# Performance work log

Hardware: AMD Instinct MI355X
Metric: run time of the kernel (lower is better)

The kernel has to match this reference:

```python
import jax, jax.numpy as jnp
import numpy as np

N = 500          # max_neurons, all alive
INPUT_SIZE = 3072
FEAT_DIM = 64
OUT_SIZE = 10
BATCH = 8192
RADIUS = 20.0
VOL = 100.0      # cubic volume (100,100,100)
N_ITER = 3


def setup_inputs() -> dict:
    key = jax.random.key(0)
    k_x, k_pos, k_iw, k_f, k_ow = jax.random.split(key, 5)
    x = jax.random.normal(k_x, (BATCH, INPUT_SIZE), dtype=jnp.float32)
    # seed positions spread across the volume, roughly matching _init_seeds
    positions = jax.random.uniform(k_pos, (N, 3), dtype=jnp.float32) * 80.0 + 10.0
    input_weights = jax.random.normal(k_iw, (N, INPUT_SIZE), dtype=jnp.float32) * 0.02
    features = jax.random.normal(k_f, (N, FEAT_DIM), dtype=jnp.float32) * 0.1
    output_weights = jax.random.normal(k_ow, (N, OUT_SIZE), dtype=jnp.float32) * 0.02
    biases = jnp.zeros((N,), dtype=jnp.float32)
    return {"x": x, "positions": positions, "input_weights": input_weights,
            "features": features, "output_weights": output_weights, "biases": biases}


def reference(x, positions, input_weights, features, output_weights, biases):
    # clamp positions into the volume (per-axis, vol is cubic here)
    pos = jnp.clip(positions, 0.1, VOL - 0.1)  # [N,3]

    # pairwise distances (grad-safe sqrt at the zero diagonal)
    diff = pos[:, None, :] - pos[None, :, :]          # [N,N,3]
    sq = jnp.sum(diff * diff, axis=-1)                # [N,N]
    pos_mask = sq > 0.0
    dist = jnp.where(pos_mask, jnp.sqrt(jnp.where(pos_mask, sq, 1.0)), 0.0)

    conn_mask = (dist < RADIUS) & (dist > 0.0)
    attenuation = jnp.exp(-dist / RADIUS) * conn_mask.astype(dist.dtype)

    # feature similarity (F.normalize clamps the norm from below at eps)
    feat_norm = features / jnp.maximum(
        jnp.linalg.norm(features, axis=1, keepdims=True), 1e-6)
    feat_sim = jnp.clip(feat_norm @ feat_norm.T, -1.0, 1.0)  # [N,N]

    conn_w = attenuation * (0.5 + 0.5 * feat_sim)
    conn_w = conn_w / (jnp.sum(conn_w, axis=1, keepdims=True) + 1e-6)

    # input gating: neurons near x=0 receive input
    x_norm = pos[:, 0] / VOL                          # [N]
    input_weight = jnp.exp(-2.0 * x_norm)
    input_weight = input_weight / (jnp.sum(input_weight) + 1e-6)

    activations = x @ input_weights.T * input_weight + biases  # [B,N]

    # iterative message passing (fixed small iteration count)
    for _ in range(N_ITER):
        msg = activations @ conn_w.T                  # [B,N]
        activations = jnp.minimum(jax.nn.relu(activations + 0.5 * msg), 50.0)

    # output gating: neurons near x=VOL emit output
    output_weight = jnp.exp(2.0 * (x_norm - 1.0))
    output_weight = output_weight / (jnp.sum(output_weight) + 1e-6)

    return activations @ (output_weights * output_weight[:, None])  # [B,OUT]
```

## Files before the change

### kernel.cpp

```cpp
#include <hip/hip_runtime.h>
#include <stdint.h>

#define N_REAL 500
#define NPAD   512
#define K_IN   3072
#define NBATCH 8192
#define NOUT   10
#define RADIUS 20.0f
#define VOLF   100.0f

typedef __attribute__((ext_vector_type(8))) __bf16 bf16x8;
typedef __attribute__((ext_vector_type(4))) float  f32x4;
typedef __attribute__((ext_vector_type(4))) unsigned short us4;

__device__ __forceinline__ unsigned short f2bf(float f) {
    unsigned int u = __float_as_uint(f);
    u += 0x7FFFu + ((u >> 16) & 1u);
    return (unsigned short)(u >> 16);
}
__device__ __forceinline__ float bf2f(unsigned short h) {
    return __uint_as_float(((unsigned int)h) << 16);
}
__device__ __forceinline__ uint2 cvt_pk4(float4 v) {
    uint2 r;
    asm("v_cvt_pk_bf16_f32 %0, %1, %2" : "=v"(r.x) : "v"(v.x), "v"(v.y));
    asm("v_cvt_pk_bf16_f32 %0, %1, %2" : "=v"(r.y) : "v"(v.z), "v"(v.w));
    return r;
}

#define GLOBAL_AS __attribute__((address_space(1)))
#define LDS_AS    __attribute__((address_space(3)))
__device__ __forceinline__ void glds16(const void* g, void* l) {
    __builtin_amdgcn_global_load_lds((const GLOBAL_AS void*)g, (LDS_AS void*)l, 16, 0, 0);
}

__global__ void prep1(const float* __restrict__ positions,
                      const float* __restrict__ features,
                      const float* __restrict__ out_w,
                      const float* __restrict__ biases,
                      float* __restrict__ feat_norm,
                      float* __restrict__ pos_c,
                      float* __restrict__ inw,
                      float* __restrict__ biasp,
                      float* __restrict__ wout)
{
    int n = threadIdx.x;
    float e_in = 0.f, e_out = 0.f;
    float px = 0.f, py = 0.f, pz = 0.f;
    if (n < N_REAL) {
        px = fminf(fmaxf(positions[n*3+0], 0.1f), VOLF - 0.1f);
        py = fminf(fmaxf(positions[n*3+1], 0.1f), VOLF - 0.1f);
        pz = fminf(fmaxf(positions[n*3+2], 0.1f), VOLF - 0.1f);
        float xn = px / VOLF;
        e_in  = expf(-2.f * xn);
        e_out = expf(2.f * (xn - 1.f));
        float ss = 0.f;
        for (int f = 0; f < 64; ++f) { float v = features[n*64+f]; ss += v*v; }
        float nm = fmaxf(sqrtf(ss), 1e-6f);
        for (int f = 0; f < 64; ++f) feat_norm[n*64+f] = features[n*64+f] / nm;
    } else {
        for (int f = 0; f < 64; ++f) feat_norm[n*64+f] = 0.f;
    }
    pos_c[n*4+0] = px; pos_c[n*4+1] = py; pos_c[n*4+2] = pz; pos_c[n*4+3] = 0.f;

    __shared__ float s_in[512], s_out[512];
    s_in[n] = e_in; s_out[n] = e_out;
    __syncthreads();
    for (int s = 256; s > 0; s >>= 1) {
        if (n < s) { s_in[n] += s_in[n+s]; s_out[n] += s_out[n+s]; }
        __syncthreads();
    }
    float sum_in  = s_in[0]  + 1e-6f;
    float sum_out = s_out[0] + 1e-6f;

    inw[n]   = (n < N_REAL) ? (e_in / sum_in) : 0.f;
    biasp[n] = (n < N_REAL) ? biases[n] : 0.f;
    float wo = (n < N_REAL) ? (e_out / sum_out) : 0.f;
    for (int o = 0; o < NOUT; ++o)
        wout[n*NOUT + o] = (n < N_REAL) ? out_w[n*NOUT + o] * wo : 0.f;
}

__global__ void prep2(const float* __restrict__ pos_c,
                      const float* __restrict__ feat_norm,
                      unsigned short* __restrict__ conn_w)
{
    int i = blockIdx.x;
    int t = threadIdx.x;
    __shared__ float fi[64];
    __shared__ float spos[4];
    __shared__ float red[128];
    if (t < 64) fi[t] = feat_norm[i*64 + t];
    if (t < 4)  spos[t] = pos_c[i*4 + t];
    __syncthreads();

    float w[4];
    float part = 0.f;
    for (int jj = 0; jj < 4; ++jj) {
        int j = t + jj*128;
        float val = 0.f;
        if (i < N_REAL && j < N_REAL) {
            float dx = spos[0] - pos_c[j*4+0];
            float dy = spos[1] - pos_c[j*4+1];
            float dz = spos[2] - pos_c[j*4+2];
            float sq = dx*dx + dy*dy + dz*dz;
            if (sq > 0.f) {
                float dist = sqrtf(sq);
                if (dist < RADIUS) {
                    float att = expf(-dist / RADIUS);
                    float sim = 0.f;
                    const float4* fj = (const float4*)(feat_norm + j*64);
                    const float4* fi4 = (const float4*)fi;
                    #pragma unroll
                    for (int f = 0; f < 16; ++f) {
                        float4 a = fi4[f]; float4 b = fj[f];
                        sim += a.x*b.x + a.y*b.y + a.z*b.z + a.w*b.w;
                    }
                    sim = fminf(fmaxf(sim, -1.f), 1.f);
                    val = att * (0.5f + 0.5f*sim);
                }
            }
        }
        w[jj] = val; part += val;
    }
    red[t] = part;
    __syncthreads();
    for (int s = 64; s > 0; s >>= 1) {
        if (t < s) red[t] += red[t+s];
        __syncthreads();
    }
    float inv = 1.f / (red[0] + 1e-6f);
    for (int jj = 0; jj < 4; ++jj)
        conn_w[(long)i*NPAD + t + jj*128] = f2bf(w[jj] * inv);
}

__global__ void cast_pad(const float* __restrict__ src, unsigned short* __restrict__ dst,
                         long total_q, long src_q)
{
    long i = (long)blockIdx.x * blockDim.x + threadIdx.x;
    long stride = (long)gridDim.x * blockDim.x;
    for (; i < total_q; i += stride) {
        us4 o;
        if (i < src_q) {
            float4 v = ((const float4*)src)[i];
            o[0] = f2bf(v.x); o[1] = f2bf(v.y); o[2] = f2bf(v.z); o[3] = f2bf(v.w);
        } else {
            o[0] = 0; o[1] = 0; o[2] = 0; o[3] = 0;
        }
        ((us4*)dst)[i] = o;
    }
}

__device__ __forceinline__ void block_map_g1(int b, int& m0, int& n0) {
    int xcd = b & 7, loc = b >> 3;
    m0 = (xcd*16 + (loc >> 3)) * 64;
    n0 = (loc & 7) * 64;
}
__device__ __forceinline__ void block_map_g2(int b, int& m0, int& n0) {
    int xcd = b & 7, loc = b >> 3;
    m0 = (xcd*16 + (loc >> 2)) * 64;
    n0 = (loc & 3) * 128;
}

__global__ __launch_bounds__(256)
void gemm1s(const float* __restrict__ X,
            const unsigned short* __restrict__ B,
            float* __restrict__ Pf)
{
    __shared__ unsigned short As[64*64];
    __shared__ unsigned short Bs[64*64];

    const int tid  = threadIdx.x;
    const int lane = tid & 63;
    const int wave = tid >> 6;
    const int bs   = blockIdx.x & 1023;
    const int ks   = blockIdx.x >> 10;
    const int kbase = ks * (K_IN/2);
    int m0, n0; block_map_g1(bs, m0, n0);
    const int wm = (wave >> 1) * 32;
    const int wn = (wave & 1) * 32;

    f32x4 acc[2][2];
    #pragma unroll
    for (int i = 0; i < 2; ++i)
        #pragma unroll
        for (int j = 0; j < 2; ++j)
            acc[i][j] = (f32x4){0.f,0.f,0.f,0.f};

    const float4* gA[4]; int lAo[4];
    #pragma unroll
    for (int s = 0; s < 4; ++s) {
        int f = tid + s*256;
        int row = f >> 4, c4 = f & 15;
        gA[s] = (const float4*)(X + (long)(m0 + row) * K_IN + kbase) + c4;
        lAo[s] = row*128 + ((c4*8) ^ ((row & 7) << 4));
    }
    const char* gB[2]; char* lB[2];
    #pragma unroll
    for (int s = 0; s < 2; ++s) {
        int o = tid*16 + s*4096;
        int row = o >> 7, d = o & 127;
        gB[s] = (const char*)B + (long)(n0 + row) * (K_IN*2) + kbase*2 + (d ^ ((row & 7) << 4));
        lB[s] = (char*)Bs + o;
    }

    for (int t = 0; t < 24; ++t) {
        __syncthreads();
        glds16(gB[0], lB[0]);
        glds16(gB[1], lB[1]);
        gB[0] += 128; gB[1] += 128;
        float4 v[4];
        #pragma unroll
        for (int s = 0; s < 4; ++s) { v[s] = gA[s][0]; gA[s] += 16; }
        #pragma unroll
        for (int s = 0; s < 4; ++s)
            *(uint2*)((char*)As + lAo[s]) = cvt_pk4(v[s]);
        asm volatile("s_waitcnt vmcnt(0) lgkmcnt(0)" ::: "memory");
        __syncthreads();

        #pragma unroll
        for (int kk = 0; kk < 2; ++kk) {
            const int cb = kk*64 + (lane >> 4) * 16;
            bf16x8 afr[2], bfr[2];
            #pragma unroll
            for (int i = 0; i < 2; ++i) {
                int r = wm + i*16 + (lane & 15);
                afr[i] = *(const bf16x8*)((const char*)As + r*128 + (cb ^ ((r & 7) << 4)));
            }
            #pragma unroll
            for (int j = 0; j < 2; ++j) {
                int r = wn + j*16 + (lane & 15);
                bfr[j] = *(const bf16x8*)((const char*)Bs + r*128 + (cb ^ ((r & 7) << 4)));
            }
            #pragma unroll
            for (int i = 0; i < 2; ++i)
                #pragma unroll
                for (int j = 0; j < 2; ++j)
                    acc[i][j] = __builtin_amdgcn_mfma_f32_16x16x32_bf16(afr[i], bfr[j], acc[i][j], 0, 0, 0);
        }
    }

    float* P = Pf + (long)ks * (NBATCH * (long)NPAD);
    const int mbase = m0 + wm + (lane >> 4) * 4;
    const int nbase = n0 + wn + (lane & 15);
    #pragma unroll
    for (int j = 0; j < 2; ++j) {
        const int n = nbase + j*16;
        #pragma unroll
        for (int i = 0; i < 2; ++i)
            #pragma unroll
            for (int r = 0; r < 4; ++r) {
                const long m = mbase + i*16 + r;
                P[m*NPAD + n] = acc[i][j][r];
            }
    }
}

__global__ __launch_bounds__(256)
void reduce_ep(const float* __restrict__ Pf,
               const float* __restrict__ inw,
               const float* __restrict__ biasp,
               unsigned short* __restrict__ act)
{
    const long TOTQ = (long)NBATCH * NPAD / 4;
    long i = (long)blockIdx.x * blockDim.x + threadIdx.x;
    long stride = (long)gridDim.x * blockDim.x;
    for (; i < TOTQ; i += stride) {
        float4 a = ((const float4*)Pf)[i];
        float4 b = ((const float4*)Pf)[i + TOTQ];
        int nq = (int)(i & 127);
        float4 w  = ((const float4*)inw)[nq];
        float4 bi = ((const float4*)biasp)[nq];
        us4 o;
        o[0] = f2bf((a.x + b.x) * w.x + bi.x);
        o[1] = f2bf((a.y + b.y) * w.y + bi.y);
        o[2] = f2bf((a.z + b.z) * w.z + bi.z);
        o[3] = f2bf((a.w + b.w) * w.w + bi.w);
        ((us4*)act)[i] = o;
    }
}

__global__ __launch_bounds__(256, 4)
void gemm2_pipe(const unsigned short* __restrict__ A,
                const unsigned short* __restrict__ B,
                unsigned short* __restrict__ Cbf,
                const unsigned short* __restrict__ actOld)
{
    constexpr int ABUF = 8192;
    constexpr int BBUF = 16384;
    __shared__ __align__(16) char lds[3*(ABUF+BBUF)];
    char* const Abase = lds;
    char* const Bbase = lds + 3*ABUF;

    const int tid  = threadIdx.x;
    const int lane = tid & 63;
    const int wave = tid >> 6;
    int m0, n0; block_map_g2(blockIdx.x, m0, n0);
    const int wm = (wave >> 1) * 32;
    const int wn = (wave & 1) * 64;

    f32x4 acc[2][4];
    #pragma unroll
    for (int i = 0; i < 2; ++i)
        #pragma unroll
        for (int j = 0; j < 4; ++j)
            acc[i][j] = (f32x4){0.f,0.f,0.f,0.f};

    const char* gB[4]; int lBo[4];
    #pragma unroll
    for (int s = 0; s < 4; ++s) {
        int o = tid*16 + s*4096;
        int row = o >> 7, d = o & 127;
        gB[s] = (const char*)B + (long)(n0 + row) * (NPAD*2) + (d ^ ((row & 7) << 4));
        lBo[s] = o;
    }
    const char* gA1[2]; int lAo1[2];
    #pragma unroll
    for (int s = 0; s < 2; ++s) {
        int o = tid*16 + s*4096;
        int row = o >> 7, d = o & 127;
        gA1[s] = (const char*)A + (long)(m0 + row) * (NPAD*2) + (d ^ ((row & 7) << 4));
        lAo1[s] = o;
    }

    const int NT = NPAD >> 6;

    #pragma unroll
    for (int s = 0; s < 2; ++s) { glds16(gA1[s], Abase + 0*ABUF + lAo1[s]); gA1[s] += 128; }
    #pragma unroll
    for (int s = 0; s < 4; ++s) { glds16(gB[s], Bbase + 0*BBUF + lBo[s]); gB[s] += 128; }
    #pragma unroll
    for (int s = 0; s < 2; ++s) { glds16(gA1[s], Abase + 1*ABUF + lAo1[s]); gA1[s] += 128; }
    #pragma unroll
    for (int s = 0; s < 4; ++s) { glds16(gB[s], Bbase + 1*BBUF + lBo[s]); gB[s] += 128; }

    int cur = 0;
    for (int t = 0; t < NT; ++t) {
        int fb = cur + 2; if (fb >= 3) fb -= 3;
        const bool more2 = (t + 2 < NT);
        const bool more1 = (t + 1 < NT);
        if (more2) {
            #pragma unroll
            for (int s = 0; s < 2; ++s) { glds16(gA1[s], Abase + fb*ABUF + lAo1[s]); gA1[s] += 128; }
            #pragma unroll
            for (int s = 0; s < 4; ++s) { glds16(gB[s], Bbase + fb*BBUF + lBo[s]); gB[s] += 128; }
            asm volatile("s_waitcnt vmcnt(12)" ::: "memory");
        } else if (more1) {
            asm volatile("s_waitcnt vmcnt(6)" ::: "memory");
        } else {
            asm volatile("s_waitcnt vmcnt(0)" ::: "memory");
        }
        __builtin_amdgcn_s_barrier();

        const char* Ab = Abase + cur*ABUF;
        const char* Bb = Bbase + cur*BBUF;
        #pragma unroll
        for (int kk = 0; kk < 2; ++kk) {
            const int cb = kk*64 + (lane >> 4) * 16;
            bf16x8 afr[2], bfr[4];
            #pragma unroll
            for (int i = 0; i < 2; ++i) {
                int r = wm + i*16 + (lane & 15);
                afr[i] = *(const bf16x8*)(Ab + r*128 + (cb ^ ((r & 7) << 4)));
            }
            #pragma unroll
            for (int j = 0; j < 4; ++j) {
                int r = wn + j*16 + (lane & 15);
                bfr[j] = *(const bf16x8*)(Bb + r*128 + (cb ^ ((r & 7) << 4)));
            }
            #pragma unroll
            for (int i = 0; i < 2; ++i)
                #pragma unroll
                for (int j = 0; j < 4; ++j)
                    acc[i][j] = __builtin_amdgcn_mfma_f32_16x16x32_bf16(afr[i], bfr[j], acc[i][j], 0, 0, 0);
        }
        __builtin_amdgcn_s_barrier();
        cur = (cur == 2) ? 0 : cur + 1;
    }

    const int mbase = m0 + wm + (lane >> 4) * 4;
    const int nbase = n0 + wn + (lane & 15);
    #pragma unroll
    for (int j = 0; j < 4; ++j) {
        const int n = nbase + j*16;
        #pragma unroll
        for (int i = 0; i < 2; ++i)
            #pragma unroll
            for (int r = 0; r < 4; ++r) {
                const long m = mbase + i*16 + r;
                float old = bf2f(actOld[m*NPAD + n]);
                float vv = fminf(fmaxf(old + 0.5f * acc[i][j][r], 0.f), 50.f);
                Cbf[m*NPAD + n] = f2bf(vv);
            }
    }
}

__global__ __launch_bounds__(256)
void out_gemm(const unsigned short* __restrict__ act,
              const float* __restrict__ wout,
              float* __restrict__ out)
{
    __shared__ float sw[NPAD * NOUT];
    const int tid = threadIdx.x;
    for (int i = tid; i < NPAD*NOUT; i += 256) sw[i] = wout[i];
    __syncthreads();

    const int lane = tid & 63;
    const int wv   = tid >> 6;
    const int row  = blockIdx.x * 4 + wv;

    const unsigned short* ap = act + (long)row * NPAD + lane * 8;
    us4 v0 = *(const us4*)(ap);
    us4 v1 = *(const us4*)(ap + 4);

    float p[NOUT];
    #pragma unroll
    for (int o = 0; o < NOUT; ++o) p[o] = 0.f;

    const int nb = lane * 8;
    #pragma unroll
    for (int e = 0; e < 8; ++e) {
        float a = bf2f(e < 4 ? v0[e] : v1[e-4]);
        const float* wr = &sw[(nb + e) * NOUT];
        #pragma unroll
        for (int o = 0; o < NOUT; ++o) p[o] += a * wr[o];
    }
    #pragma unroll
    for (int o = 0; o < NOUT; ++o) {
        float s = p[o];
        for (int d = 32; d > 0; d >>= 1) s += __shfl_down(s, d);
        if (lane == 0) out[(long)row * NOUT + o] = s;
    }
}

extern "C" void kernel_launch(void* const* d_in, const int* in_sizes, int n_in,
                              void* d_out, int out_size, void* d_ws, size_t ws_size,
                              hipStream_t stream)
{
    const float* x        = (const float*)d_in[0];
    const float* pos      = (const float*)d_in[1];
    const float* in_w     = (const float*)d_in[2];
    const float* feats    = (const float*)d_in[3];
    const float* out_w    = (const float*)d_in[4];
    const float* biases   = (const float*)d_in[5];
    float* out = (float*)d_out;

    char* ws = (char*)d_ws;
    unsigned short* iw_bf  = (unsigned short*)(ws);
    unsigned short* connw  = (unsigned short*)(ws + 3145728);
    unsigned short* act_a  = (unsigned short*)(ws + 3670016);
    unsigned short* act_b  = (unsigned short*)(ws + 12058624);
    float* feat_norm = (float*)(ws + 20447232);
    float* pos_c     = (float*)(ws + 20578304);
    float* inw       = (float*)(ws + 20586496);
    float* biasp     = (float*)(ws + 20588544);
    float* wout      = (float*)(ws + 20590592);
    float* partials  = (float*)(ws + 20611072);

    prep1<<<1, 512, 0, stream>>>(pos, feats, out_w, biases, feat_norm, pos_c, inw, biasp, wout);
    prep2<<<512, 128, 0, stream>>>(pos_c, feat_norm, connw);
    cast_pad<<<512, 256, 0, stream>>>(in_w, iw_bf, 393216L, 384000L);

    gemm1s<<<2048, 256, 0, stream>>>(x, iw_bf, partials);
    reduce_ep<<<2048, 256, 0, stream>>>(partials, inw, biasp, act_a);

    gemm2_pipe<<<512, 256, 0, stream>>>(act_a, connw, act_b, act_a);
    gemm2_pipe<<<512, 256, 0, stream>>>(act_b, connw, act_a, act_b);
    gemm2_pipe<<<512, 256, 0, stream>>>(act_a, connw, act_b, act_a);

    out_gemm<<<NBATCH/4, 256, 0, stream>>>(act_b, wout, out);
}
```

Baseline: 131.7 us.

## Enlarge input GEMM tiles to 128x128 and switch to 4-way split-K

Each gemm1s block now computes a 128x128 output tile with a 4x4 MFMA accumulator per wave, and split-K goes from 2 to 4 slices. The block mapping now spreads the K slices across blocks, and reduce_ep sums four partial buffers instead of two. The goal is to cut redundant fp32 reads of X, which are now shared by 4 N-blocks instead of 8, and to raise MFMA work per LDS load. In exchange the partial buffers double in size, adding write and reduce traffic, and register pressure rises under a 4-blocks-per-CU launch bound.

Result: slower. 136.7 us (+3.8%).

```diff
diff --git a/kernel.cpp b/kernel.cpp
--- a/kernel.cpp
+++ b/kernel.cpp
@@ -150,10 +150,12 @@
     }
 }
 
-__device__ __forceinline__ void block_map_g1(int b, int& m0, int& n0) {
+__device__ __forceinline__ void block_map_g1(int b, int& m0, int& n0, int& ks) {
     int xcd = b & 7, loc = b >> 3;
-    m0 = (xcd*16 + (loc >> 3)) * 64;
-    n0 = (loc & 7) * 64;
+    m0 = (xcd*8 + (loc >> 4)) * 128;
+    int rest = loc & 15;
+    n0 = (rest & 3) * 128;
+    ks = rest >> 2;
 }
 __device__ __forceinline__ void block_map_g2(int b, int& m0, int& n0) {
     int xcd = b & 7, loc = b >> 3;
@@ -161,80 +163,82 @@
     n0 = (loc & 3) * 128;
 }
 
-__global__ __launch_bounds__(256)
+__global__ __launch_bounds__(256, 4)
 void gemm1s(const float* __restrict__ X,
             const unsigned short* __restrict__ B,
             float* __restrict__ Pf)
 {
-    __shared__ unsigned short As[64*64];
-    __shared__ unsigned short Bs[64*64];
+    __shared__ unsigned short As[128*64];
+    __shared__ unsigned short Bs[128*64];
 
     const int tid  = threadIdx.x;
     const int lane = tid & 63;
     const int wave = tid >> 6;
-    const int bs   = blockIdx.x & 1023;
-    const int ks   = blockIdx.x >> 10;
-    const int kbase = ks * (K_IN/2);
-    int m0, n0; block_map_g1(bs, m0, n0);
-    const int wm = (wave >> 1) * 32;
-    const int wn = (wave & 1) * 32;
-
-    f32x4 acc[2][2];
-    #pragma unroll
-    for (int i = 0; i < 2; ++i)
-        #pragma unroll
-        for (int j = 0; j < 2; ++j)
+    int m0, n0, ks; block_map_g1(blockIdx.x, m0, n0, ks);
+    const int kbase = ks * (K_IN/4);
+    const int wm = (wave >> 1) * 64;
+    const int wn = (wave & 1) * 64;
+
+    f32x4 acc[4][4];
+    #pragma unroll
+    for (int i = 0; i < 4; ++i)
+        #pragma unroll
+        for (int j = 0; j < 4; ++j)
             acc[i][j] = (f32x4){0.f,0.f,0.f,0.f};
 
-    const float4* gA[4]; int lAo[4];
-    #pragma unroll
-    for (int s = 0; s < 4; ++s) {
+    const float4* gA[8]; int lAo[8];
+    #pragma unroll
+    for (int s = 0; s < 8; ++s) {
         int f = tid + s*256;
         int row = f >> 4, c4 = f & 15;
         gA[s] = (const float4*)(X + (long)(m0 + row) * K_IN + kbase) + c4;
         lAo[s] = row*128 + ((c4*8) ^ ((row & 7) << 4));
     }
-    const char* gB[2]; char* lB[2];
-    #pragma unroll
-    for (int s = 0; s < 2; ++s) {
+    const char* gB[4]; char* lB[4];
+    #pragma unroll
+    for (int s = 0; s < 4; ++s) {
         int o = tid*16 + s*4096;
         int row = o >> 7, d = o & 127;
         gB[s] = (const char*)B + (long)(n0 + row) * (K_IN*2) + kbase*2 + (d ^ ((row & 7) << 4));
         lB[s] = (char*)Bs + o;
     }
 
-    for (int t = 0; t < 24; ++t) {
+    for (int t = 0; t < 12; ++t) {
         __syncthreads();
-        glds16(gB[0], lB[0]);
-        glds16(gB[1], lB[1]);
-        gB[0] += 128; gB[1] += 128;
-        float4 v[4];
-        #pragma unroll
-        for (int s = 0; s < 4; ++s) { v[s] = gA[s][0]; gA[s] += 16; }
+        float4 va[4], vb4[4];
+        #pragma unroll
+        for (int s = 0; s < 4; ++s) { va[s] = gA[s][0]; gA[s] += 16; }
+        #pragma unroll
+        for (int s = 0; s < 4; ++s) { glds16(gB[s], lB[s]); gB[s] += 128; }
+        #pragma unroll
+        for (int s = 4; s < 8; ++s) { vb4[s-4] = gA[s][0]; gA[s] += 16; }
         #pragma unroll
         for (int s = 0; s < 4; ++s)
-            *(uint2*)((char*)As + lAo[s]) = cvt_pk4(v[s]);
+            *(uint2*)((char*)As + lAo[s]) = cvt_pk4(va[s]);
+        #pragma unroll
+        for (int s = 4; s < 8; ++s)
+            *(uint2*)((char*)As + lAo[s]) = cvt_pk4(vb4[s-4]);
         asm volatile("s_waitcnt vmcnt(0) lgkmcnt(0)" ::: "memory");
         __syncthreads();
 
         #pragma unroll
         for (int kk = 0; kk < 2; ++kk) {
             const int cb = kk*64 + (lane >> 4) * 16;
-            bf16x8 afr[2], bfr[2];
-            #pragma unroll
-            for (int i = 0; i < 2; ++i) {
+            bf16x8 afr[4], bfr[4];
+            #pragma unroll
+            for (int i = 0; i < 4; ++i) {
                 int r = wm + i*16 + (lane & 15);
                 afr[i] = *(const bf16x8*)((const char*)As + r*128 + (cb ^ ((r & 7) << 4)));
             }
             #pragma unroll
-            for (int j = 0; j < 2; ++j) {
+            for (int j = 0; j < 4; ++j) {
                 int r = wn + j*16 + (lane & 15);
                 bfr[j] = *(const bf16x8*)((const char*)Bs + r*128 + (cb ^ ((r & 7) << 4)));
             }
             #pragma unroll
-            for (int i = 0; i < 2; ++i)
+            for (int i = 0; i < 4; ++i)
                 #pragma unroll
-                for (int j = 0; j < 2; ++j)
+                for (int j = 0; j < 4; ++j)
                     acc[i][j] = __builtin_amdgcn_mfma_f32_16x16x32_bf16(afr[i], bfr[j], acc[i][j], 0, 0, 0);
         }
     }
@@ -243,10 +247,10 @@
     const int mbase = m0 + wm + (lane >> 4) * 4;
     const int nbase = n0 + wn + (lane & 15);
     #pragma unroll
-    for (int j = 0; j < 2; ++j) {
+    for (int j = 0; j < 4; ++j) {
         const int n = nbase + j*16;
         #pragma unroll
-        for (int i = 0; i < 2; ++i)
+        for (int i = 0; i < 4; ++i)
             #pragma unroll
             for (int r = 0; r < 4; ++r) {
                 const long m = mbase + i*16 + r;
@@ -267,14 +271,16 @@
     for (; i < TOTQ; i += stride) {
         float4 a = ((const float4*)Pf)[i];
         float4 b = ((const float4*)Pf)[i + TOTQ];
+        float4 c = ((const float4*)Pf)[i + 2*TOTQ];
+        float4 d = ((const float4*)Pf)[i + 3*TOTQ];
         int nq = (int)(i & 127);
         float4 w  = ((const float4*)inw)[nq];
         float4 bi = ((const float4*)biasp)[nq];
         us4 o;
-        o[0] = f2bf((a.x + b.x) * w.x + bi.x);
-        o[1] = f2bf((a.y + b.y) * w.y + bi.y);
-        o[2] = f2bf((a.z + b.z) * w.z + bi.z);
-        o[3] = f2bf((a.w + b.w) * w.w + bi.w);
+        o[0] = f2bf((((a.x + b.x) + c.x) + d.x) * w.x + bi.x);
+        o[1] = f2bf((((a.y + b.y) + c.y) + d.y) * w.y + bi.y);
+        o[2] = f2bf((((a.z + b.z) + c.z) + d.z) * w.z + bi.z);
+        o[3] = f2bf((((a.w + b.w) + c.w) + d.w) * w.w + bi.w);
         ((us4*)act)[i] = o;
     }
 }
@@ -460,7 +466,7 @@
     prep2<<<512, 128, 0, stream>>>(pos_c, feat_norm, connw);
     cast_pad<<<512, 256, 0, stream>>>(in_w, iw_bf, 393216L, 384000L);
 
-    gemm1s<<<2048, 256, 0, stream>>>(x, iw_bf, partials);
+    gemm1s<<<1024, 256, 0, stream>>>(x, iw_bf, partials);
     reduce_ep<<<2048, 256, 0, stream>>>(partials, inw, biasp, act_a);
 
     gemm2_pipe<<<512, 256, 0, stream>>>(act_a, connw, act_b, act_a);
```
